# Kernel tuning notes

Measured on AMD Instinct MI355X. Metric: run time of the kernel, lower is better.

The kernel has to match this reference:

```python
import jax, jax.numpy as jnp
import numpy as np
from jax import lax


def _conv(x, w, b):
    y = lax.conv_general_dilated(x, w, window_strides=(1, 1), padding='SAME',
                                 dimension_numbers=('NCHW', 'OIHW', 'NCHW'))
    return y + b[None, :, None, None]


def _maxpool2(x):
    return lax.reduce_window(x, -jnp.inf, lax.max,
                             window_dimensions=(1, 1, 2, 2),
                             window_strides=(1, 1, 2, 2), padding='VALID')


def setup_inputs() -> dict:
    key = jax.random.key(0)
    ks = jax.random.split(key, 11)
    f32 = jnp.float32
    return {
        'x': jax.random.normal(ks[0], (512, 1, 112, 112), f32),
        'w_conv1': jax.random.normal(ks[1], (8, 1, 3, 3), f32) * 0.1,
        'b_conv1': jax.random.normal(ks[2], (8,), f32) * 0.1,
        'w_conv2': jax.random.normal(ks[3], (16, 8, 3, 3), f32) * 0.1,
        'b_conv2': jax.random.normal(ks[4], (16,), f32) * 0.1,
        'w_patch': jax.random.normal(ks[5], (4, 64), f32) * 0.1,
        'b_patch': jax.random.normal(ks[6], (4,), f32) * 0.1,
        'w_fc1': jax.random.normal(ks[7], (64, 784), f32) * 0.05,
        'b_fc1': jax.random.normal(ks[8], (64,), f32) * 0.05,
        'w_fc2': jax.random.normal(ks[9], (10, 64), f32) * 0.05,
        'b_fc2': jax.random.normal(ks[10], (10,), f32) * 0.05,
    }


def reference(x, w_conv1, b_conv1, w_conv2, b_conv2, w_patch, b_patch,
              w_fc1, b_fc1, w_fc2, b_fc2):
    B = x.shape[0]
    h = _maxpool2(jax.nn.relu(_conv(x, w_conv1, b_conv1)))        # [B,8,56,56]
    f = _maxpool2(jax.nn.relu(_conv(h, w_conv2, b_conv2)))        # [B,16,28,28]
    C, H, W = f.shape[1], f.shape[2], f.shape[3]
    # im2col: 2x2 non-overlapping spatial patches, flattened as (C,2,2) -> 64
    p = f.reshape(B, C, H // 2, 2, W // 2, 2)
    p = p.transpose(0, 2, 4, 1, 3, 5).reshape(B, (H // 2) * (W // 2), C * 4)  # [B,196,64]
    pf = jnp.einsum('bpk,ok->bpo', p, w_patch) + b_patch          # [B,196,4]
    pf = pf.reshape(B, -1)                                        # [B,784]
    h1 = jax.nn.relu(pf @ w_fc1.T + b_fc1)
    logits = h1 @ w_fc2.T + b_fc2
    return jax.nn.log_softmax(logits, axis=-1)
```

## Files before the change

kernel.cpp:

```cpp
#include <hip/hip_runtime.h>


#define HSTR 36
#define NROWS 30
#define FSTR 33

typedef _Float16 half2_t __attribute__((ext_vector_type(2)));
typedef _Float16 f16x8 __attribute__((ext_vector_type(8)));
typedef float f32x4 __attribute__((ext_vector_type(4)));
typedef float f32x2 __attribute__((ext_vector_type(2)));

__device__ __forceinline__ unsigned pack_f16(float a, float b) {
  union { half2_t h; unsigned u; } z;
  z.h[0] = (_Float16)a;
  z.h[1] = (_Float16)b;
  return z.u;
}

__device__ __forceinline__ half2_t as_h2(unsigned u) {
  union { unsigned u; half2_t h; } z;
  z.u = u;
  return z.h;
}

__device__ __forceinline__ f16x8 as_f16x8(uint4 u) {
  union { uint4 u; f16x8 f; } z;
  z.u = u;
  return z.f;
}

__device__ __forceinline__ float fdot2_(half2_t a, half2_t b, float c) {
#if __has_builtin(__builtin_amdgcn_fdot2)
  return __builtin_amdgcn_fdot2(a, b, c, false);
#else
  return c + (float)a[0] * (float)b[0] + (float)a[1] * (float)b[1];
#endif
}

__global__ __launch_bounds__(256, 5) void k_fused(
    const float* __restrict__ x, const float* __restrict__ w1,
    const float* __restrict__ b1, const float* __restrict__ w2,
    const float* __restrict__ b2, const float* __restrict__ wp,
    const float* __restrict__ bp, const float* __restrict__ w_fc1,
    float* __restrict__ h1p) {
  __shared__ __align__(16) unsigned hsu[4 * NROWS * HSTR];
  __shared__ __align__(16) unsigned bwl[768];
  __shared__ __align__(16) unsigned wps[128];
  __shared__ __align__(16) unsigned fsu[49 * FSTR];
  __shared__ __align__(16) float pfl[196];
  const int tid = threadIdx.x;
  const int b = blockIdx.x >> 2;
  const int tile = blockIdx.x & 3;
  const int sr = tile >> 1;
  const int sc = tile & 1;
  const int l = tid & 63;
  const int wv = __builtin_amdgcn_readfirstlane(tid >> 6);
  const float* xb = x + (long)b * 12544;
  const float bpv = bp[tid & 3];

  for (int i = tid; i < 4 * NROWS * HSTR; i += 256) hsu[i] = 0u;
  for (int t = tid; t < 768; t += 256) {
    int oc = t / 48, k32 = t % 48;
    unsigned v = 0u;
    if (k32 < 36) {
      int icp = k32 / 9, tap = k32 - icp * 9;
      v = pack_f16(w2[(oc * 8 + 2 * icp) * 9 + tap],
                   w2[(oc * 8 + 2 * icp + 1) * 9 + tap]);
    }
    bwl[t] = v;
  }
  if (tid < 128) {
    int i = tid >> 2, ot = tid & 3;
    int l0 = 2 * i, l1 = 2 * i + 1;
    wps[tid] = pack_f16(wp[ot * 64 + (l0 & 15) * 4 + (l0 >> 4)],
                        wp[ot * 64 + (l1 & 15) * 4 + (l1 >> 4)]);
  }
  __syncthreads();

  for (int task = tid; task < 900; task += 256) {
    int r = task / 30, c = task - r * 30;
    int gr = 28 * sr - 1 + r;
    int gc = 28 * sc - 1 + c;
    if ((unsigned)gr >= 56u || (unsigned)gc >= 56u) continue;
    float win[4][4];
    int iy0 = 2 * gr - 1, ix0 = 2 * gc - 1;
    if (gr >= 1 && gr <= 54 && gc >= 1 && gc <= 54) {
      const float* xp = xb + iy0 * 112 + ix0;
#pragma unroll
      for (int rr = 0; rr < 4; ++rr)
#pragma unroll
        for (int qq = 0; qq < 4; ++qq)
          win[rr][qq] = xp[rr * 112 + qq];
    } else {
#pragma unroll
      for (int rr = 0; rr < 4; ++rr) {
        int iy = iy0 + rr;
        bool yok = (unsigned)iy < 112u;
#pragma unroll
        for (int qq = 0; qq < 4; ++qq) {
          int ix = ix0 + qq;
          win[rr][qq] = (yok && (unsigned)ix < 112u) ? xb[iy * 112 + ix] : 0.f;
        }
      }
    }
    float hv[8];
#pragma unroll
    for (int ch = 0; ch < 8; ++ch) {
      f32x2 sA = {0.f, 0.f};
      f32x2 sB = {0.f, 0.f};
#pragma unroll
      for (int ty = 0; ty < 3; ++ty)
#pragma unroll
        for (int tx = 0; tx < 3; ++tx) {
          float wk = w1[ch * 9 + ty * 3 + tx];
          f32x2 wkk = {wk, wk};
          f32x2 xa = {win[ty][tx], win[ty][tx + 1]};
          f32x2 xb2 = {win[ty + 1][tx], win[ty + 1][tx + 1]};
          sA = __builtin_elementwise_fma(xa, wkk, sA);
          sB = __builtin_elementwise_fma(xb2, wkk, sB);
        }
      f32x2 sm = __builtin_elementwise_max(sA, sB);
      float m = fmaxf(sm.x, sm.y);
      hv[ch] = fmaxf(m + b1[ch], 0.f);
    }
#pragma unroll
    for (int cp = 0; cp < 4; ++cp)
      hsu[(cp * NROWS + r) * HSTR + c] = pack_f16(hv[2 * cp], hv[2 * cp + 1]);
  }
  __syncthreads();

  {
    const int q = l >> 4;
    int offs[12];
#pragma unroll
    for (int kk = 0; kk < 3; ++kk)
#pragma unroll
      for (int i = 0; i < 4; ++i) {
        int k32 = kk * 16 + q * 4 + i;
        int icp = k32 / 9, tap = k32 - icp * 9;
        int ty = tap / 3, tx = tap - ty * 3;
        offs[kk * 4 + i] = (icp * NROWS + ty) * HSTR + tx;
      }
    const int yoff = 2 * ((l >> 3) & 1) + ((l >> 1) & 1);
    const int xoff = 2 * ((l >> 2) & 1) + (l & 1);
    uint4 bu0 = *(const uint4*)(bwl + (l & 15) * 48 + 0 * 16 + q * 4);
    uint4 bu1 = *(const uint4*)(bwl + (l & 15) * 48 + 1 * 16 + q * 4);
    uint4 bu2 = *(const uint4*)(bwl + (l & 15) * 48 + 2 * 16 + q * 4);
    const float b2v = b2[l & 15];
    _Float16* fsh = (_Float16*)fsu;

#pragma unroll 2
    for (int p_l = wv; p_l < 49; p_l += 4) {
      int py = p_l / 7, px = p_l - py * 7;
      int base = (4 * py + yoff) * HSTR + 4 * px + xoff;
      uint4 a0u, a1u, a2u = make_uint4(0u, 0u, 0u, 0u);
      a0u.x = hsu[base + offs[0]];
      a0u.y = hsu[base + offs[1]];
      a0u.z = hsu[base + offs[2]];
      a0u.w = hsu[base + offs[3]];
      a1u.x = hsu[base + offs[4]];
      a1u.y = hsu[base + offs[5]];
      a1u.z = hsu[base + offs[6]];
      a1u.w = hsu[base + offs[7]];
      if (q == 0) {
        a2u.x = hsu[base + offs[8]];
        a2u.y = hsu[base + offs[9]];
        a2u.z = hsu[base + offs[10]];
        a2u.w = hsu[base + offs[11]];
      }
      f32x4 acc = {0.f, 0.f, 0.f, 0.f};
      acc = __builtin_amdgcn_mfma_f32_16x16x32_f16(as_f16x8(a0u), as_f16x8(bu0), acc, 0, 0, 0);
      acc = __builtin_amdgcn_mfma_f32_16x16x32_f16(as_f16x8(a1u), as_f16x8(bu1), acc, 0, 0, 0);
      acc = __builtin_amdgcn_mfma_f32_16x16x32_f16(as_f16x8(a2u), as_f16x8(bu2), acc, 0, 0, 0);
      float mx = fmaxf(fmaxf(acc[0], acc[1]), fmaxf(acc[2], acc[3]));
      float fv = fmaxf(mx + b2v, 0.f);
      fsh[p_l * (2 * FSTR) + l] = (_Float16)fv;
    }
    __syncthreads();
    if (tid < 196) {
      int row = tid >> 2, ot = tid & 3;
      const unsigned* fr = fsu + row * FSTR;
      float acc = 0.f;
#pragma unroll
      for (int i = 0; i < 32; ++i)
        acc = fdot2_(as_h2(fr[i]), as_h2(wps[i * 4 + ot]), acc);
      pfl[row * 4 + ot] = acc + bpv;
    }
    __syncthreads();
  }

  {
    int j = tid >> 2, q4 = tid & 3;
    const float* wrow = w_fc1 + j * 784;
    float acc = 0.f;
#pragma unroll 4
    for (int lp = q4; lp < 49; lp += 4) {
      int Pl = lp / 7, Ql = lp - Pl * 7;
      int gp = (7 * sr + Pl) * 14 + 7 * sc + Ql;
      float4 w4 = *(const float4*)(wrow + gp * 4);
      float4 p4 = *(const float4*)(pfl + lp * 4);
      acc += w4.x * p4.x + w4.y * p4.y + w4.z * p4.z + w4.w * p4.w;
    }
    acc += __shfl_down(acc, 2, 4);
    acc += __shfl_down(acc, 1, 4);
    if (q4 == 0) h1p[((long)b * 4 + tile) * 64 + j] = acc;
  }
}

__global__ __launch_bounds__(256) void k_tail(const float* __restrict__ h1p,
                                              const float* __restrict__ b_fc1,
                                              const float* __restrict__ w_fc2,
                                              const float* __restrict__ b_fc2,
                                              float* __restrict__ out) {
  const int l = threadIdx.x & 63;
  const int wv = threadIdx.x >> 6;
  const int b = blockIdx.x * 4 + wv;
  const float* hp = h1p + (long)b * 256;
  float v = b_fc1[l] + hp[l] + hp[64 + l] + hp[128 + l] + hp[192 + l];
  float h = fmaxf(v, 0.f);
  float lg[10];
#pragma unroll
  for (int o = 0; o < 10; ++o) {
    float t = h * w_fc2[o * 64 + l];
#pragma unroll
    for (int off = 32; off; off >>= 1) t += __shfl_xor(t, off);
    lg[o] = t + b_fc2[o];
  }
  float mx = lg[0];
#pragma unroll
  for (int o = 1; o < 10; ++o) mx = fmaxf(mx, lg[o]);
  float se = 0.f;
#pragma unroll
  for (int o = 0; o < 10; ++o) se += __expf(lg[o] - mx);
  float ls = mx + __logf(se);
#pragma unroll
  for (int o = 0; o < 10; ++o)
    if (l == o) out[b * 10 + o] = lg[o] - ls;
}

extern "C" void kernel_launch(void* const* d_in, const int* in_sizes, int n_in,
                              void* d_out, int out_size, void* d_ws, size_t ws_size,
                              hipStream_t stream) {
  const float* x = (const float*)d_in[0];
  const float* w1 = (const float*)d_in[1];
  const float* b1 = (const float*)d_in[2];
  const float* w2 = (const float*)d_in[3];
  const float* b2 = (const float*)d_in[4];
  const float* wp = (const float*)d_in[5];
  const float* bp = (const float*)d_in[6];
  const float* wf1 = (const float*)d_in[7];
  const float* bf1 = (const float*)d_in[8];
  const float* wf2 = (const float*)d_in[9];
  const float* bf2 = (const float*)d_in[10];

  float* h1p = (float*)d_ws;

  k_fused<<<dim3(2048), 256, 0, stream>>>(x, w1, b1, w2, b2, wp, bp, wf1, h1p);
  k_tail<<<dim3(128), 256, 0, stream>>>(h1p, bf1, wf2, bf2, (float*)d_out);
}
```

Before: 121.5 us.

## Store conv1 output channel-interleaved so MFMA A-operands load as single 16-byte reads

The conv1 activation tile in shared memory moves from a channel-pair-planar layout to a pixel-major layout with all 8 channels packed in one 16-byte word. The K dimension of the conv2 MFMA is reordered to tap-major, so each A fragment becomes one vector LDS read instead of four scalar reads, and the stores become one vector write per pixel. The conv2 weights are reordered to match, and the padded K slots reuse a clamped tap whose weights are zero. The smaller LDS footprint lets launch bounds request 6 waves per EU, which may pressure registers and LDS bank conflicts on the 16-byte accesses.

```diff
diff --git a/kernel.cpp b/kernel.cpp
--- a/kernel.cpp
+++ b/kernel.cpp
@@ -1,8 +1,6 @@
 #include <hip/hip_runtime.h>
 
 
-#define HSTR 36
-#define NROWS 30
 #define FSTR 33
 
 typedef _Float16 half2_t __attribute__((ext_vector_type(2)));
@@ -37,13 +35,13 @@
 #endif
 }
 
-__global__ __launch_bounds__(256, 5) void k_fused(
+__global__ __launch_bounds__(256, 6) void k_fused(
     const float* __restrict__ x, const float* __restrict__ w1,
     const float* __restrict__ b1, const float* __restrict__ w2,
     const float* __restrict__ b2, const float* __restrict__ wp,
     const float* __restrict__ bp, const float* __restrict__ w_fc1,
     float* __restrict__ h1p) {
-  __shared__ __align__(16) unsigned hsu[4 * NROWS * HSTR];
+  __shared__ __align__(16) unsigned hsu[3600];
   __shared__ __align__(16) unsigned bwl[768];
   __shared__ __align__(16) unsigned wps[128];
   __shared__ __align__(16) unsigned fsu[49 * FSTR];
@@ -58,15 +56,14 @@
   const float* xb = x + (long)b * 12544;
   const float bpv = bp[tid & 3];
 
-  for (int i = tid; i < 4 * NROWS * HSTR; i += 256) hsu[i] = 0u;
+  for (int i = tid; i < 3600; i += 256) hsu[i] = 0u;
   for (int t = tid; t < 768; t += 256) {
-    int oc = t / 48, k32 = t % 48;
+    int oc = t / 48, rem = t - oc * 48;
+    int tap = rem >> 2, w = rem & 3;
     unsigned v = 0u;
-    if (k32 < 36) {
-      int icp = k32 / 9, tap = k32 - icp * 9;
-      v = pack_f16(w2[(oc * 8 + 2 * icp) * 9 + tap],
-                   w2[(oc * 8 + 2 * icp + 1) * 9 + tap]);
-    }
+    if (tap < 9)
+      v = pack_f16(w2[(oc * 8 + 2 * w) * 9 + tap],
+                   w2[(oc * 8 + 2 * w + 1) * 9 + tap]);
     bwl[t] = v;
   }
   if (tid < 128) {
@@ -123,51 +120,40 @@
       float m = fmaxf(sm.x, sm.y);
       hv[ch] = fmaxf(m + b1[ch], 0.f);
     }
-#pragma unroll
-    for (int cp = 0; cp < 4; ++cp)
-      hsu[(cp * NROWS + r) * HSTR + c] = pack_f16(hv[2 * cp], hv[2 * cp + 1]);
+    uint4 hw;
+    hw.x = pack_f16(hv[0], hv[1]);
+    hw.y = pack_f16(hv[2], hv[3]);
+    hw.z = pack_f16(hv[4], hv[5]);
+    hw.w = pack_f16(hv[6], hv[7]);
+    *(uint4*)(hsu + (r * 30 + c) * 4) = hw;
   }
   __syncthreads();
 
   {
     const int q = l >> 4;
-    int offs[12];
-#pragma unroll
-    for (int kk = 0; kk < 3; ++kk)
-#pragma unroll
-      for (int i = 0; i < 4; ++i) {
-        int k32 = kk * 16 + q * 4 + i;
-        int icp = k32 / 9, tap = k32 - icp * 9;
-        int ty = tap / 3, tx = tap - ty * 3;
-        offs[kk * 4 + i] = (icp * NROWS + ty) * HSTR + tx;
-      }
     const int yoff = 2 * ((l >> 3) & 1) + ((l >> 1) & 1);
     const int xoff = 2 * ((l >> 2) & 1) + (l & 1);
-    uint4 bu0 = *(const uint4*)(bwl + (l & 15) * 48 + 0 * 16 + q * 4);
-    uint4 bu1 = *(const uint4*)(bwl + (l & 15) * 48 + 1 * 16 + q * 4);
-    uint4 bu2 = *(const uint4*)(bwl + (l & 15) * 48 + 2 * 16 + q * 4);
+    int poff[3];
+#pragma unroll
+    for (int kk = 0; kk < 3; ++kk) {
+      int t = kk * 4 + q;
+      int tt = t < 9 ? t : 8;
+      int ty = tt / 3, tx = tt - ty * 3;
+      poff[kk] = ((yoff + ty) * 30 + xoff + tx) * 4;
+    }
+    uint4 bu0 = *(const uint4*)(bwl + ((l & 15) * 12 + 0 + q) * 4);
+    uint4 bu1 = *(const uint4*)(bwl + ((l & 15) * 12 + 4 + q) * 4);
+    uint4 bu2 = *(const uint4*)(bwl + ((l & 15) * 12 + 8 + q) * 4);
     const float b2v = b2[l & 15];
     _Float16* fsh = (_Float16*)fsu;
 
 #pragma unroll 2
     for (int p_l = wv; p_l < 49; p_l += 4) {
       int py = p_l / 7, px = p_l - py * 7;
-      int base = (4 * py + yoff) * HSTR + 4 * px + xoff;
-      uint4 a0u, a1u, a2u = make_uint4(0u, 0u, 0u, 0u);
-      a0u.x = hsu[base + offs[0]];
-      a0u.y = hsu[base + offs[1]];
-      a0u.z = hsu[base + offs[2]];
-      a0u.w = hsu[base + offs[3]];
-      a1u.x = hsu[base + offs[4]];
-      a1u.y = hsu[base + offs[5]];
-      a1u.z = hsu[base + offs[6]];
-      a1u.w = hsu[base + offs[7]];
-      if (q == 0) {
-        a2u.x = hsu[base + offs[8]];
-        a2u.y = hsu[base + offs[9]];
-        a2u.z = hsu[base + offs[10]];
-        a2u.w = hsu[base + offs[11]];
-      }
+      int pb = 480 * py + 16 * px;
+      uint4 a0u = *(const uint4*)(hsu + pb + poff[0]);
+      uint4 a1u = *(const uint4*)(hsu + pb + poff[1]);
+      uint4 a2u = *(const uint4*)(hsu + pb + poff[2]);
       f32x4 acc = {0.f, 0.f, 0.f, 0.f};
       acc = __builtin_amdgcn_mfma_f32_16x16x32_f16(as_f16x8(a0u), as_f16x8(bu0), acc, 0, 0, 0);
       acc = __builtin_amdgcn_mfma_f32_16x16x32_f16(as_f16x8(a1u), as_f16x8(bu1), acc, 0, 0, 0);
```

Result: faster. 117.8 us (-3.1%).
